# Performance work log

Hardware: AMD Instinct MI355X
Metric: run time of the kernel (lower is better)

The kernel has to match this reference:

```python
import jax, jax.numpy as jnp
import numpy as np

T, BATCH, DMODEL, H = 2048, 16, 512, 512


def setup_inputs() -> dict:
    key = jax.random.key(0)
    ks = jax.random.split(key, 8)
    x = jax.random.normal(ks[0], (T, BATCH, DMODEL), jnp.float32)
    # initial carry: (lambda=1, h=0) so the concat trick leaves state untouched
    h0_re = jnp.zeros((1, BATCH, H), jnp.float32)
    h0_im = jnp.zeros((1, BATCH, H), jnp.float32)
    # LRU parameterization (Orvieto et al. 2023): |lambda| in [0.9, 0.99]
    u1 = jax.random.uniform(ks[1], (H,), jnp.float32)
    nu_log = jnp.log(-0.5 * jnp.log(u1 * (0.99 ** 2 - 0.9 ** 2) + 0.9 ** 2))
    theta_log = jnp.log(jax.random.uniform(ks[2], (H,), jnp.float32) * (np.pi / 10) + 1e-4)
    B_re = jax.random.normal(ks[3], (H, DMODEL), jnp.float32) / np.sqrt(2 * DMODEL)
    B_im = jax.random.normal(ks[4], (H, DMODEL), jnp.float32) / np.sqrt(2 * DMODEL)
    C_re = jax.random.normal(ks[5], (DMODEL, H), jnp.float32) / np.sqrt(H)
    C_im = jax.random.normal(ks[6], (DMODEL, H), jnp.float32) / np.sqrt(H)
    D_vec = jax.random.normal(ks[7], (DMODEL,), jnp.float32)
    return dict(x=x, h0_re=h0_re, h0_im=h0_im, nu_log=nu_log, theta_log=theta_log,
                B_re=B_re, B_im=B_im, C_re=C_re, C_im=C_im, D_vec=D_vec)


def _binop(qi, qj):
    # associative combine for h_t = a_t * h_{t-1} + b_t
    a_i, b_i = qi
    a_j, b_j = qj
    return (a_j * a_i, a_j * b_i + b_j)


def reference(x, h0_re, h0_im, nu_log, theta_log, B_re, B_im, C_re, C_im, D_vec):
    # diagonal complex recurrence eigenvalues, |Lambda| = exp(-exp(nu_log)) < 1
    Lam = jnp.exp(-jnp.exp(nu_log) + 1j * jnp.exp(theta_log))        # [H] complex64
    gamma = jnp.sqrt(1.0 - jnp.exp(-2.0 * jnp.exp(nu_log)))           # [H]
    Bmat = (B_re + 1j * B_im) * gamma[:, None]                         # [H, D]
    # map_to_h: Bu elements and broadcast Lambda elements
    Bu = jnp.einsum('tbd,hd->tbh', x.astype(jnp.complex64), Bmat)      # [T, B, H]
    Lam_el = jnp.broadcast_to(Lam, Bu.shape)                            # [T, B, H]
    # concat previous state (lambda=1, b=h0) as first scan element
    h0 = (h0_re + 1j * h0_im).astype(jnp.complex64)                    # [1, B, H]
    a = jnp.concatenate([jnp.ones_like(h0), Lam_el], axis=0)          # [T+1, B, H]
    b = jnp.concatenate([h0, Bu], axis=0)                              # [T+1, B, H]
    _, h_all = jax.lax.associative_scan(_binop, (a, b), axis=0)
    h = h_all[1:]                                                       # [T, B, H]
    # map_from_h: y = Re(C h) + D * x (elementwise skip)
    Cmat = C_re + 1j * C_im                                             # [D, H]
    y = jnp.einsum('tbh,dh->tbd', h, Cmat).real + D_vec * x            # [T, B, D]
    final_state = h[-1:]                                                # [1, B, H]
    return (final_state, y)
```

## Files before the change

### kernel.cpp

```cpp
#include <hip/hip_runtime.h>
#include <stdint.h>

typedef short shortx8 __attribute__((ext_vector_type(8)));
typedef float floatx4 __attribute__((ext_vector_type(4)));

#define T_LEN 2048
#define BATCH 16
#define DMODEL 512
#define HDIM 512
#define M_ROWS (T_LEN * BATCH)
#define NCHUNK 32
#define LCHUNK 64
#define NCHAIN (BATCH * HDIM)
#define Y_ELEMS (M_ROWS * DMODEL)

__device__ __forceinline__ unsigned short f2bf(float f) {
    union { float f; unsigned u; } v; v.f = f;
    unsigned r = (v.u + 0x7FFFu + ((v.u >> 16) & 1u)) >> 16;
    return (unsigned short)r;
}
__device__ __forceinline__ float bf2f(unsigned short u) {
    union { unsigned u; float f; } v; v.u = ((unsigned)u) << 16;
    return v.f;
}

__global__ void prep_kernel(const float* __restrict__ nu_log, const float* __restrict__ th_log,
                            float* lam_re, float* lam_im, float* l64_re, float* l64_im, float* gam) {
    int h = blockIdx.x * blockDim.x + threadIdx.x;
    if (h >= HDIM) return;
    double nu  = exp((double)nu_log[h]);
    double th  = exp((double)th_log[h]);
    double mag = exp(-nu);
    double lre = mag * cos(th), lim = mag * sin(th);
    double g   = sqrt(1.0 - exp(-2.0 * nu));
    double zr = lre, zi = lim;
    for (int i = 0; i < 6; ++i) { double nr = zr*zr - zi*zi; zi = 2.0*zr*zi; zr = nr; }
    lam_re[h] = (float)lre; lam_im[h] = (float)lim;
    l64_re[h] = (float)zr;  l64_im[h] = (float)zi;
    gam[h] = (float)g;
}

__global__ void conv_B_kernel(const float* __restrict__ B_re, const float* __restrict__ B_im,
                              const float* __restrict__ gam, unsigned short* __restrict__ Bs) {
    int idx = blockIdx.x * blockDim.x + threadIdx.x;
    int n = idx >> 9;
    int d = idx & 511;
    int h = n & 511;
    float v = (n < HDIM ? B_re[h * DMODEL + d] : B_im[h * DMODEL + d]) * gam[h];
    Bs[idx] = f2bf(v);
}

__global__ void conv_C_kernel(const float* __restrict__ C_re, const float* __restrict__ C_im,
                              unsigned short* __restrict__ C2) {
    int idx = blockIdx.x * blockDim.x + threadIdx.x;
    int d = idx >> 10;
    int k = idx & 1023;
    float v = (k < HDIM) ? C_re[d * HDIM + k] : -C_im[d * HDIM + (k - HDIM)];
    C2[idx] = f2bf(v);
}

__global__ void cast_x_kernel(const float4* __restrict__ x4, unsigned short* __restrict__ xb, int n4) {
    int i = blockIdx.x * blockDim.x + threadIdx.x;
    if (i >= n4) return;
    float4 v = x4[i];
    ushort4 u;
    u.x = f2bf(v.x); u.y = f2bf(v.y); u.z = f2bf(v.z); u.w = f2bf(v.w);
    *(ushort4*)(xb + (size_t)i * 4) = u;
}

template <int MODE>
__global__ __launch_bounds__(256) void gemm_nt(const unsigned short* __restrict__ A,
                                               const unsigned short* __restrict__ Bmat,
                                               const int K, const int N,
                                               unsigned short* __restrict__ OutB,
                                               float* __restrict__ OutF,
                                               const float* __restrict__ Dv,
                                               const float* __restrict__ Xf) {
    __shared__ unsigned short As[128 * 32];
    __shared__ unsigned short Bs[128 * 32];
    const int bm = blockIdx.x, bn = blockIdx.y;
    const int tid = threadIdx.x;
    const int wv = tid >> 6, lane = tid & 63;
    const int wr = wv >> 1, wc = wv & 1;
    const int lrow = lane & 15, qq = lane >> 4;
    floatx4 acc[4][4] = {};

    const size_t rowA = (size_t)bm * 128, rowB = (size_t)bn * 128;
    for (int k0 = 0; k0 < K; k0 += 32) {
        #pragma unroll
        for (int j = 0; j < 2; ++j) {
            int chunk = j * 256 + wv * 64 + lane;
            int r  = chunk >> 2;
            int cc = (chunk & 3) * 8;
            const unsigned short* ga = A    + (rowA + r) * (size_t)K + (k0 + cc);
            const unsigned short* gb = Bmat + (rowB + r) * (size_t)K + (k0 + cc);
            unsigned short* la = As + (size_t)(j * 256 + wv * 64) * 8;
            unsigned short* lb = Bs + (size_t)(j * 256 + wv * 64) * 8;
            __builtin_amdgcn_global_load_lds((const __attribute__((address_space(1))) void*)ga,
                                             (__attribute__((address_space(3))) void*)la, 16, 0, 0);
            __builtin_amdgcn_global_load_lds((const __attribute__((address_space(1))) void*)gb,
                                             (__attribute__((address_space(3))) void*)lb, 16, 0, 0);
        }
        __syncthreads();
        shortx8 af[4], bf[4];
        #pragma unroll
        for (int mi = 0; mi < 4; ++mi)
            af[mi] = *(const shortx8*)&As[(wr * 64 + mi * 16 + lrow) * 32 + qq * 8];
        #pragma unroll
        for (int ni = 0; ni < 4; ++ni)
            bf[ni] = *(const shortx8*)&Bs[(wc * 64 + ni * 16 + lrow) * 32 + qq * 8];
        #pragma unroll
        for (int mi = 0; mi < 4; ++mi)
            #pragma unroll
            for (int ni = 0; ni < 4; ++ni)
                acc[mi][ni] = __builtin_amdgcn_mfma_f32_16x16x32_bf16(af[mi], bf[ni], acc[mi][ni], 0, 0, 0);
        __syncthreads();
    }

    #pragma unroll
    for (int mi = 0; mi < 4; ++mi) {
        int mbase = bm * 128 + wr * 64 + mi * 16 + qq * 4;
        #pragma unroll
        for (int ni = 0; ni < 4; ++ni) {
            int n = bn * 128 + wc * 64 + ni * 16 + lrow;
            if (MODE == 0) {
                #pragma unroll
                for (int r = 0; r < 4; ++r)
                    OutB[(size_t)(mbase + r) * N + n] = f2bf(acc[mi][ni][r]);
            } else {
                float dv = Dv[n];
                #pragma unroll
                for (int r = 0; r < 4; ++r) {
                    size_t idx = (size_t)(mbase + r) * N + n;
                    OutF[idx] = acc[mi][ni][r] + dv * Xf[idx];
                }
            }
        }
    }
}

__global__ void scan_partial(const unsigned short* __restrict__ Bu,
                             const float* __restrict__ lam_re, const float* __restrict__ lam_im,
                             float* __restrict__ car_re, float* __restrict__ car_im) {
    int gid = blockIdx.x * blockDim.x + threadIdx.x;
    int chunk = gid >> 13;
    int c = gid & (NCHAIN - 1);
    int b = c >> 9, h = c & 511;
    float lre = lam_re[h], lim = lam_im[h];
    float vre = 0.f, vim = 0.f;
    const unsigned short* p = Bu + (size_t)chunk * LCHUNK * BATCH * 1024 + (size_t)b * 1024 + h;
    for (int j = 0; j < LCHUNK; ++j) {
        float br = bf2f(p[0]), bi = bf2f(p[512]);
        float nr = lre * vre - lim * vim + br;
        float ni = lre * vim + lim * vre + bi;
        vre = nr; vim = ni;
        p += BATCH * 1024;
    }
    car_re[chunk * NCHAIN + c] = vre;
    car_im[chunk * NCHAIN + c] = vim;
}

__global__ void scan_combine(const float* __restrict__ car_re, const float* __restrict__ car_im,
                             const float* __restrict__ l64_re, const float* __restrict__ l64_im,
                             const float* __restrict__ h0_re, const float* __restrict__ h0_im,
                             float* __restrict__ cin_re, float* __restrict__ cin_im,
                             float* __restrict__ out_final, int interleave) {
    int c = blockIdx.x * blockDim.x + threadIdx.x;
    int h = c & 511;
    float lre = l64_re[h], lim = l64_im[h];
    float vre = h0_re[c], vim = h0_im[c];
    for (int k = 0; k < NCHUNK; ++k) {
        cin_re[k * NCHAIN + c] = vre;
        cin_im[k * NCHAIN + c] = vim;
        float cr = car_re[k * NCHAIN + c], ci = car_im[k * NCHAIN + c];
        float nr = lre * vre - lim * vim + cr;
        float ni = lre * vim + lim * vre + ci;
        vre = nr; vim = ni;
    }
    if (interleave) {
        out_final[2 * c]     = vre;
        out_final[2 * c + 1] = vim;
    } else {
        out_final[c] = vre;
    }
}

__global__ void scan_apply(unsigned short* __restrict__ Bu,
                           const float* __restrict__ lam_re, const float* __restrict__ lam_im,
                           const float* __restrict__ cin_re, const float* __restrict__ cin_im) {
    int gid = blockIdx.x * blockDim.x + threadIdx.x;
    int chunk = gid >> 13;
    int c = gid & (NCHAIN - 1);
    int b = c >> 9, h = c & 511;
    float lre = lam_re[h], lim = lam_im[h];
    float vre = cin_re[chunk * NCHAIN + c], vim = cin_im[chunk * NCHAIN + c];
    unsigned short* p = Bu + (size_t)chunk * LCHUNK * BATCH * 1024 + (size_t)b * 1024 + h;
    for (int j = 0; j < LCHUNK; ++j) {
        float br = bf2f(p[0]), bi = bf2f(p[512]);
        float nr = lre * vre - lim * vim + br;
        float ni = lre * vim + lim * vre + bi;
        vre = nr; vim = ni;
        p[0]   = f2bf(vre);
        p[512] = f2bf(vim);
        p += BATCH * 1024;
    }
}

extern "C" void kernel_launch(void* const* d_in, const int* in_sizes, int n_in,
                              void* d_out, int out_size, void* d_ws, size_t ws_size,
                              hipStream_t stream) {
    const float* x        = (const float*)d_in[0];
    const float* h0_re    = (const float*)d_in[1];
    const float* h0_im    = (const float*)d_in[2];
    const float* nu_log   = (const float*)d_in[3];
    const float* theta_lg = (const float*)d_in[4];
    const float* B_re     = (const float*)d_in[5];
    const float* B_im     = (const float*)d_in[6];
    const float* C_re     = (const float*)d_in[7];
    const float* C_im     = (const float*)d_in[8];
    const float* D_vec    = (const float*)d_in[9];

    char* ws = (char*)d_ws;
    unsigned short* BuH  = (unsigned short*)(ws + 0);
    unsigned short* xb   = (unsigned short*)(ws + 67108864);
    unsigned short* Bs   = (unsigned short*)(ws + 100663296);
    unsigned short* C2   = (unsigned short*)(ws + 101711872);
    float* car_re        = (float*)(ws + 102760448);
    float* car_im        = (float*)(ws + 103809024);
    float* cin_re        = (float*)(ws + 104857600);
    float* cin_im        = (float*)(ws + 105906176);
    float* lam_re        = (float*)(ws + 106954752);
    float* lam_im        = (float*)(ws + 106956800);
    float* l64_re        = (float*)(ws + 106958848);
    float* l64_im        = (float*)(ws + 106960896);
    float* gam           = (float*)(ws + 106962944);

    int fs_elems = out_size - Y_ELEMS;
    int interleave = (fs_elems == 8192) ? 0 : 1;
    if (fs_elems != 8192) fs_elems = 16384;
    float* out_final = (float*)d_out;
    float* y_out     = (float*)d_out + fs_elems;

    prep_kernel<<<2, 256, 0, stream>>>(nu_log, theta_lg, lam_re, lam_im, l64_re, l64_im, gam);
    conv_B_kernel<<<(1024 * 512) / 256, 256, 0, stream>>>(B_re, B_im, gam, Bs);
    conv_C_kernel<<<(512 * 1024) / 256, 256, 0, stream>>>(C_re, C_im, C2);
    cast_x_kernel<<<(Y_ELEMS / 4) / 256, 256, 0, stream>>>((const float4*)x, xb, Y_ELEMS / 4);
    {
        dim3 g(M_ROWS / 128, 1024 / 128);
        gemm_nt<0><<<g, 256, 0, stream>>>(xb, Bs, DMODEL, 1024, BuH, nullptr, nullptr, nullptr);
    }
    scan_partial<<<(NCHUNK * NCHAIN) / 256, 256, 0, stream>>>(BuH, lam_re, lam_im, car_re, car_im);
    scan_combine<<<NCHAIN / 256, 256, 0, stream>>>(car_re, car_im, l64_re, l64_im,
                                                   h0_re, h0_im, cin_re, cin_im, out_final, interleave);
    scan_apply<<<(NCHUNK * NCHAIN) / 256, 256, 0, stream>>>(BuH, lam_re, lam_im, cin_re, cin_im);
    {
        dim3 g(M_ROWS / 128, 512 / 128);
        gemm_nt<1><<<g, 256, 0, stream>>>(BuH, C2, 1024, 512, nullptr, y_out, D_vec, x);
    }
}
```

Baseline: 311.8 us.

## Remap GEMM blocks per XCD, vectorize scan over channel pairs, merge B/C conversion

The GEMM grid becomes 1D and is remapped so each of the 8 XCDs handles a contiguous range of 32 row-blocks across all column-blocks, so A tiles are reused in that XCD's L2. The scan kernels now handle two adjacent hidden channels per thread, using 32-bit packed bf16 loads and stores instead of 16-bit ones, which halves the thread count and widens memory accesses. The B and C weight conversions are merged into one launch. Each scan thread does more serial work, and the block mapping hardcodes M_ROWS/128=256 split as 8x32.

```diff
diff --git a/kernel.cpp b/kernel.cpp
--- a/kernel.cpp
+++ b/kernel.cpp
@@ -40,23 +40,24 @@
     gam[h] = (float)g;
 }
 
-__global__ void conv_B_kernel(const float* __restrict__ B_re, const float* __restrict__ B_im,
-                              const float* __restrict__ gam, unsigned short* __restrict__ Bs) {
+__global__ void conv_BC_kernel(const float* __restrict__ B_re, const float* __restrict__ B_im,
+                               const float* __restrict__ gam,
+                               const float* __restrict__ C_re, const float* __restrict__ C_im,
+                               unsigned short* __restrict__ Bs, unsigned short* __restrict__ C2) {
     int idx = blockIdx.x * blockDim.x + threadIdx.x;
-    int n = idx >> 9;
-    int d = idx & 511;
-    int h = n & 511;
-    float v = (n < HDIM ? B_re[h * DMODEL + d] : B_im[h * DMODEL + d]) * gam[h];
-    Bs[idx] = f2bf(v);
-}
-
-__global__ void conv_C_kernel(const float* __restrict__ C_re, const float* __restrict__ C_im,
-                              unsigned short* __restrict__ C2) {
-    int idx = blockIdx.x * blockDim.x + threadIdx.x;
-    int d = idx >> 10;
-    int k = idx & 1023;
-    float v = (k < HDIM) ? C_re[d * HDIM + k] : -C_im[d * HDIM + (k - HDIM)];
-    C2[idx] = f2bf(v);
+    if (idx < 524288) {
+        int n = idx >> 9;
+        int d = idx & 511;
+        int h = n & 511;
+        float v = (n < HDIM ? B_re[h * DMODEL + d] : B_im[h * DMODEL + d]) * gam[h];
+        Bs[idx] = f2bf(v);
+    } else {
+        int i2 = idx - 524288;
+        int d = i2 >> 10;
+        int k = i2 & 1023;
+        float v = (k < HDIM) ? C_re[d * HDIM + k] : -C_im[d * HDIM + (k - HDIM)];
+        C2[i2] = f2bf(v);
+    }
 }
 
 __global__ void cast_x_kernel(const float4* __restrict__ x4, unsigned short* __restrict__ xb, int n4) {
@@ -71,14 +72,18 @@
 template <int MODE>
 __global__ __launch_bounds__(256) void gemm_nt(const unsigned short* __restrict__ A,
                                                const unsigned short* __restrict__ Bmat,
-                                               const int K, const int N,
+                                               const int K, const int N, const int lgNB,
                                                unsigned short* __restrict__ OutB,
                                                float* __restrict__ OutF,
                                                const float* __restrict__ Dv,
                                                const float* __restrict__ Xf) {
     __shared__ unsigned short As[128 * 32];
     __shared__ unsigned short Bs[128 * 32];
-    const int bm = blockIdx.x, bn = blockIdx.y;
+    const int L = blockIdx.x;
+    const int xcd = L & 7;
+    const int slot = L >> 3;
+    const int bn = slot & ((1 << lgNB) - 1);
+    const int bm = xcd * 32 + (slot >> lgNB);
     const int tid = threadIdx.x;
     const int wv = tid >> 6, lane = tid & 63;
     const int wr = wv >> 1, wc = wv & 1;
@@ -143,21 +148,29 @@
                              const float* __restrict__ lam_re, const float* __restrict__ lam_im,
                              float* __restrict__ car_re, float* __restrict__ car_im) {
     int gid = blockIdx.x * blockDim.x + threadIdx.x;
-    int chunk = gid >> 13;
-    int c = gid & (NCHAIN - 1);
-    int b = c >> 9, h = c & 511;
-    float lre = lam_re[h], lim = lam_im[h];
-    float vre = 0.f, vim = 0.f;
+    int chunk = gid >> 12;
+    int idx = gid & 4095;
+    int b = idx >> 8, hp = idx & 255;
+    int h = hp * 2;
+    float lr0 = lam_re[h], li0 = lam_im[h];
+    float lr1 = lam_re[h + 1], li1 = lam_im[h + 1];
+    float v0r = 0.f, v0i = 0.f, v1r = 0.f, v1i = 0.f;
     const unsigned short* p = Bu + (size_t)chunk * LCHUNK * BATCH * 1024 + (size_t)b * 1024 + h;
     for (int j = 0; j < LCHUNK; ++j) {
-        float br = bf2f(p[0]), bi = bf2f(p[512]);
-        float nr = lre * vre - lim * vim + br;
-        float ni = lre * vim + lim * vre + bi;
-        vre = nr; vim = ni;
+        unsigned rr = *(const unsigned*)p;
+        unsigned ii = *(const unsigned*)(p + 512);
+        float b0r = bf2f((unsigned short)rr), b1r = bf2f((unsigned short)(rr >> 16));
+        float b0i = bf2f((unsigned short)ii), b1i = bf2f((unsigned short)(ii >> 16));
+        float n0r = lr0 * v0r - li0 * v0i + b0r;
+        float n0i = lr0 * v0i + li0 * v0r + b0i;
+        float n1r = lr1 * v1r - li1 * v1i + b1r;
+        float n1i = lr1 * v1i + li1 * v1r + b1i;
+        v0r = n0r; v0i = n0i; v1r = n1r; v1i = n1i;
         p += BATCH * 1024;
     }
-    car_re[chunk * NCHAIN + c] = vre;
-    car_im[chunk * NCHAIN + c] = vim;
+    int c = b * 512 + h;
+    *(float2*)&car_re[chunk * NCHAIN + c] = make_float2(v0r, v1r);
+    *(float2*)&car_im[chunk * NCHAIN + c] = make_float2(v0i, v1i);
 }
 
 __global__ void scan_combine(const float* __restrict__ car_re, const float* __restrict__ car_im,
@@ -189,19 +202,29 @@
                            const float* __restrict__ lam_re, const float* __restrict__ lam_im,
                            const float* __restrict__ cin_re, const float* __restrict__ cin_im) {
     int gid = blockIdx.x * blockDim.x + threadIdx.x;
-    int chunk = gid >> 13;
-    int c = gid & (NCHAIN - 1);
-    int b = c >> 9, h = c & 511;
-    float lre = lam_re[h], lim = lam_im[h];
-    float vre = cin_re[chunk * NCHAIN + c], vim = cin_im[chunk * NCHAIN + c];
+    int chunk = gid >> 12;
+    int idx = gid & 4095;
+    int b = idx >> 8, hp = idx & 255;
+    int h = hp * 2;
+    int c = b * 512 + h;
+    float lr0 = lam_re[h], li0 = lam_im[h];
+    float lr1 = lam_re[h + 1], li1 = lam_im[h + 1];
+    float2 cr = *(const float2*)&cin_re[chunk * NCHAIN + c];
+    float2 ci = *(const float2*)&cin_im[chunk * NCHAIN + c];
+    float v0r = cr.x, v0i = ci.x, v1r = cr.y, v1i = ci.y;
     unsigned short* p = Bu + (size_t)chunk * LCHUNK * BATCH * 1024 + (size_t)b * 1024 + h;
     for (int j = 0; j < LCHUNK; ++j) {
-        float br = bf2f(p[0]), bi = bf2f(p[512]);
-        float nr = lre * vre - lim * vim + br;
-        float ni = lre * vim + lim * vre + bi;
-        vre = nr; vim = ni;
-        p[0]   = f2bf(vre);
-        p[512] = f2bf(vim);
+        unsigned rr = *(const unsigned*)p;
+        unsigned ii = *(const unsigned*)(p + 512);
+        float b0r = bf2f((unsigned short)rr), b1r = bf2f((unsigned short)(rr >> 16));
+        float b0i = bf2f((unsigned short)ii), b1i = bf2f((unsigned short)(ii >> 16));
+        float n0r = lr0 * v0r - li0 * v0i + b0r;
+        float n0i = lr0 * v0i + li0 * v0r + b0i;
+        float n1r = lr1 * v1r - li1 * v1i + b1r;
+        float n1i = lr1 * v1i + li1 * v1r + b1i;
+        v0r = n0r; v0i = n0i; v1r = n1r; v1i = n1i;
+        *(unsigned*)p         = (unsigned)f2bf(v0r) | ((unsigned)f2bf(v1r) << 16);
+        *(unsigned*)(p + 512) = (unsigned)f2bf(v0i) | ((unsigned)f2bf(v1i) << 16);
         p += BATCH * 1024;
     }
 }
@@ -242,19 +265,12 @@
     float* y_out     = (float*)d_out + fs_elems;
 
     prep_kernel<<<2, 256, 0, stream>>>(nu_log, theta_lg, lam_re, lam_im, l64_re, l64_im, gam);
-    conv_B_kernel<<<(1024 * 512) / 256, 256, 0, stream>>>(B_re, B_im, gam, Bs);
-    conv_C_kernel<<<(512 * 1024) / 256, 256, 0, stream>>>(C_re, C_im, C2);
+    conv_BC_kernel<<<(1048576) / 256, 256, 0, stream>>>(B_re, B_im, gam, C_re, C_im, Bs, C2);
     cast_x_kernel<<<(Y_ELEMS / 4) / 256, 256, 0, stream>>>((const float4*)x, xb, Y_ELEMS / 4);
-    {
-        dim3 g(M_ROWS / 128, 1024 / 128);
-        gemm_nt<0><<<g, 256, 0, stream>>>(xb, Bs, DMODEL, 1024, BuH, nullptr, nullptr, nullptr);
-    }
-    scan_partial<<<(NCHUNK * NCHAIN) / 256, 256, 0, stream>>>(BuH, lam_re, lam_im, car_re, car_im);
+    gemm_nt<0><<<2048, 256, 0, stream>>>(xb, Bs, DMODEL, 1024, 3, BuH, nullptr, nullptr, nullptr);
+    scan_partial<<<(NCHUNK * NCHAIN / 2) / 256, 256, 0, stream>>>(BuH, lam_re, lam_im, car_re, car_im);
     scan_combine<<<NCHAIN / 256, 256, 0, stream>>>(car_re, car_im, l64_re, l64_im,
                                                    h0_re, h0_im, cin_re, cin_im, out_final, interleave);
-    scan_apply<<<(NCHUNK * NCHAIN) / 256, 256, 0, stream>>>(BuH, lam_re, lam_im, cin_re, cin_im);
-    {
-        dim3 g(M_ROWS / 128, 512 / 128);
-        gemm_nt<1><<<g, 256, 0, stream>>>(BuH, C2, 1024, 512, nullptr, y_out, D_vec, x);
-    }
-}
+    scan_apply<<<(NCHUNK * NCHAIN / 2) / 256, 256, 0, stream>>>(BuH, lam_re, lam_im, cin_re, cin_im);
+    gemm_nt<1><<<1024, 256, 0, stream>>>(BuH, C2, 1024, 512, 2, nullptr, y_out, D_vec, x);
+}
```

Result: faster. 291.0 us (-6.7%).
